# Kernel tuning notes

Hardware: AMD Instinct MI355X
Metric: run time of the kernel (lower is better)

Reference implementation:

```python
import jax, jax.numpy as jnp
import numpy as np

B, T, DIM = 4, 1024, 2048
N_HEADS, N_KV_HEADS = 32, 8
HEAD_DIM = DIM // N_HEADS  # 64
N_REPS = N_HEADS // N_KV_HEADS  # 4


def setup_inputs() -> dict:
    key = jax.random.key(0)
    ks = jax.random.split(key, 8)
    # RoPE tables: theta = 10000^{-2i/d}, positions 0..T-1
    inv_freq = 1.0 / (10000.0 ** (jnp.arange(0, HEAD_DIM, 2, dtype=jnp.float32) / HEAD_DIM))
    angles = jnp.arange(T, dtype=jnp.float32)[:, None] * inv_freq[None, :]  # (T, HEAD_DIM//2)
    s = 0.02
    return {
        "input": jax.random.normal(ks[0], (B, T, DIM), jnp.float32),
        "freqs_cos": jnp.cos(angles),
        "freqs_sin": jnp.sin(angles),
        "mask": jnp.tril(jnp.ones((T, T), dtype=bool)),  # causal boolean mask
        "wq": s * jax.random.normal(ks[1], (DIM, DIM), jnp.float32),
        "wk": s * jax.random.normal(ks[2], (N_KV_HEADS * HEAD_DIM, DIM), jnp.float32),
        "wv": s * jax.random.normal(ks[3], (N_KV_HEADS * HEAD_DIM, DIM), jnp.float32),
        "wo": s * jax.random.normal(ks[4], (DIM, DIM), jnp.float32),
        "curr_pos": 0,
    }


def _apply_rope(x, cos, sin):
    # x: (B, T, H, D); cos/sin: (T, D//2). Complex multiply on (even, odd) pairs.
    xr = x[..., 0::2]
    xi = x[..., 1::2]
    c = cos[None, :, None, :]
    s = sin[None, :, None, :]
    out_r = xr * c - xi * s
    out_i = xr * s + xi * c
    return jnp.stack([out_r, out_i], axis=-1).reshape(x.shape)


def reference(input, freqs_cos, freqs_sin, mask, wq, wk, wv, wo, curr_pos):
    Bv, Tv = input.shape[0], input.shape[1]
    qs = (input @ wq.T).reshape(Bv, Tv, N_HEADS, HEAD_DIM)
    ks = (input @ wk.T).reshape(Bv, Tv, N_KV_HEADS, HEAD_DIM)
    vs = (input @ wv.T).reshape(Bv, Tv, N_KV_HEADS, HEAD_DIM)
    qs = _apply_rope(qs, freqs_cos, freqs_sin)
    ks = _apply_rope(ks, freqs_cos, freqs_sin)

    # KV cache (prefill path: curr_pos == 0, fresh cache of length 2T)
    kv_cache = jnp.zeros((Bv, 2 * Tv, N_KV_HEADS, HEAD_DIM, 2), input.dtype)
    kv_cache = kv_cache.at[:, curr_pos:curr_pos + Tv, :, :, 0].set(ks)
    kv_cache = kv_cache.at[:, curr_pos:curr_pos + Tv, :, :, 1].set(vs)
    k_all = kv_cache[:, :curr_pos + Tv, :, :, 0]
    v_all = kv_cache[:, :curr_pos + Tv, :, :, 1]

    # GQA: broadcast each kv head across its query-head group (avoid repeat_interleave copy)
    S = k_all.shape[1]
    q = qs.transpose(0, 2, 1, 3).reshape(Bv, N_KV_HEADS, N_REPS, Tv, HEAD_DIM)
    k = k_all.transpose(0, 2, 1, 3)  # (B, KVH, S, D)
    v = v_all.transpose(0, 2, 1, 3)

    scale = 1.0 / jnp.sqrt(jnp.asarray(HEAD_DIM, input.dtype))
    scores = jnp.einsum("bgrqd,bgkd->bgrqk", q, k) * scale  # (B, KVH, REPS, T, S)
    neg = jnp.asarray(jnp.finfo(input.dtype).min, input.dtype)
    scores = jnp.where(mask[None, None, None, :, :S], scores, neg)
    attn = jax.nn.softmax(scores, axis=-1)
    out = jnp.einsum("bgrqk,bgkd->bgrqd", attn, v)
    out = out.reshape(Bv, N_HEADS, Tv, HEAD_DIM).transpose(0, 2, 1, 3).reshape(Bv, Tv, DIM)
    return out @ wo.T
```

## Files before the change

kernel.cpp:

```cpp
#include <hip/hip_runtime.h>
#include <cstdint>

typedef __bf16 bf16x8 __attribute__((ext_vector_type(8)));
typedef float  f32x4  __attribute__((ext_vector_type(4)));
typedef float  f32x16 __attribute__((ext_vector_type(16)));
typedef float  float8v __attribute__((ext_vector_type(8)));
typedef unsigned short ushort8v __attribute__((ext_vector_type(8)));
typedef unsigned short ushort4v __attribute__((ext_vector_type(4)));
typedef unsigned int   uint4v   __attribute__((ext_vector_type(4)));

__device__ __forceinline__ unsigned short f2b(float f) {
  uint32_t u = __builtin_bit_cast(uint32_t, f);
  u += 0x7FFFu + ((u >> 16) & 1u);
  return (unsigned short)(u >> 16);
}
__device__ __forceinline__ float b2f(unsigned short h) {
  uint32_t u = ((uint32_t)h) << 16;
  return __builtin_bit_cast(float, u);
}
__device__ __forceinline__ unsigned int cvtpk(float lo, float hi_) {
  unsigned int r;
  asm("v_cvt_pk_bf16_f32 %0, %1, %2" : "=v"(r) : "v"(lo), "v"(hi_));
  return r;
}

__device__ __forceinline__ void async16(const void* g, void* l) {
  __builtin_amdgcn_global_load_lds(
      (const __attribute__((address_space(1))) void*)g,
      (__attribute__((address_space(3))) void*)l, 16, 0, 0);
}

#define WAITVM(N)  __builtin_amdgcn_s_waitcnt(0x0F70 | ((N) & 15))
#define WAITLGKM0  __builtin_amdgcn_s_waitcnt(0xC07F)

struct CvtArgs {
  const float* src[5];
  unsigned short* dst[5];
  long n[5];
};
__global__ void cvt5_kernel(CvtArgs a) {
  long base = (long)blockIdx.x * blockDim.x + threadIdx.x;
  long gstride = (long)gridDim.x * blockDim.x;
#pragma unroll 1
  for (int sg = 0; sg < 5; ++sg) {
    const float* s = a.src[sg];
    unsigned short* d = a.dst[sg];
    long n8 = a.n[sg] >> 3;
    for (long i = base; i < n8; i += gstride) {
      float8v f = *(const float8v*)(s + i * 8);
      ushort8v o;
#pragma unroll
      for (int j = 0; j < 8; ++j) o[j] = f2b(f[j]);
      *(ushort8v*)(d + i * 8) = o;
    }
  }
}

template<bool F32OUT, int BN, int GX>
__global__ __launch_bounds__(512, 1)
void gemm8p(const unsigned short* __restrict__ Ag, const unsigned short* __restrict__ Wg,
            void* __restrict__ Cp, int M, int N) {
  constexpr int K = 2048;
  constexpr int NF = BN / 64;
  constexpr int BL = BN / 128;
  constexpr int VN = 4 + 2 * BL;
  constexpr int VT1 = (BN == 256) ? 6 : 4;
  constexpr int VT2 = (BN == 256) ? 4 : 3;
  constexpr int VT3 = (BN == 256) ? 2 : 1;
  constexpr int ASLOT = 16384;
  constexpr int BSLOT = BN * 64;
  constexpr int CPX = 2 * GX;

  extern __shared__ char lds_c[];

  const int tid = threadIdx.x;
  const int wave = tid >> 6, lane = tid & 63;
  const int wm = wave >> 2, wn = wave & 3;
  const int lr = lane & 15, lg = lane >> 4;

  const int flat = blockIdx.y * GX + blockIdx.x;
  const int swz = (flat & 7) * CPX + (flat >> 3);
  const int m0 = (swz / GX) * 256, n0 = (swz % GX) * BN;

  const int laneSw = (lr >> 1) * 128 + (((((lr & 1) << 2) | lg) ^ (lr >> 1)) << 4);
  const int aoff = wm * 8192 + laneSw;
  const int boff = wn * NF * 1024 + laneSw;

  f32x4 acc[8][NF] = {};

  auto stageHT = [&](int s) {
    const int ty = s & 3;
    const int kh = (s >> 1) & 1;
    const int buf = (s >> 2) & 1;
    const int kc = (s >> 2) * 64 + kh * 32;
    if (ty == 0 || ty == 2) {
      char* slot = lds_c + (buf * 2 + kh) * ASLOT;
#pragma unroll
      for (int j = 0; j < 2; ++j) {
        int q = (tid + 512 * j) * 16;
        int R = q >> 7, g2L = ((q >> 4) & 7) ^ (R & 7);
        int row = R * 2 + (g2L >> 2), kg = g2L & 3;
        async16(Ag + (size_t)(m0 + row) * K + kc + kg * 8, slot + q);
      }
    } else {
      char* slot = lds_c + 65536 + (buf * 2 + kh) * BSLOT;
#pragma unroll
      for (int j = 0; j < BL; ++j) {
        int q = (tid + 512 * j) * 16;
        int R = q >> 7, g2L = ((q >> 4) & 7) ^ (R & 7);
        int row = R * 2 + (g2L >> 2), kg = g2L & 3;
        async16(Wg + (size_t)(n0 + row) * K + kc + kg * 8, slot + q);
      }
    }
  };

#define PHASE(BUF, KH, MH, VM, ...)                                           \
  {                                                                           \
    const char* As_ = lds_c + ((BUF) * 2 + (KH)) * ASLOT;                     \
    const char* Bs_ = lds_c + 65536 + ((BUF) * 2 + (KH)) * BSLOT;             \
    bf16x8 af_[4], bf_[NF];                                                   \
    _Pragma("unroll") for (int mi = 0; mi < 4; ++mi)                          \
      af_[mi] = *(const bf16x8*)(As_ + aoff + (MH) * 4096 + mi * 1024);       \
    _Pragma("unroll") for (int ni = 0; ni < NF; ++ni)                         \
      bf_[ni] = *(const bf16x8*)(Bs_ + boff + ni * 1024);                     \
    __VA_ARGS__;                                                              \
    WAITVM(VM);                                                               \
    __builtin_amdgcn_s_barrier();                                             \
    WAITLGKM0;                                                                \
    __builtin_amdgcn_sched_barrier(0);                                        \
    __builtin_amdgcn_s_setprio(1);                                            \
    _Pragma("unroll") for (int mi = 0; mi < 4; ++mi)                          \
      _Pragma("unroll") for (int ni = 0; ni < NF; ++ni)                       \
        acc[(MH) * 4 + mi][ni] = __builtin_amdgcn_mfma_f32_16x16x32_bf16(     \
            af_[mi], bf_[ni], acc[(MH) * 4 + mi][ni], 0, 0, 0);               \
    __builtin_amdgcn_s_setprio(0);                                            \
    __builtin_amdgcn_s_barrier();                                             \
  }

#pragma unroll
  for (int s = 0; s < 6; ++s) stageHT(s);
  WAITVM(VN);
  __builtin_amdgcn_s_barrier();

#pragma unroll 2
  for (int kt = 0; kt < 30; ++kt) {
    const int buf = kt & 1;
    const int s0 = kt * 4 + 6;
    PHASE(buf, 0, 0, VN, stageHT(s0));
    PHASE(buf, 0, 1, VN, stageHT(s0 + 1));
    PHASE(buf, 1, 0, VN, stageHT(s0 + 2));
    PHASE(buf, 1, 1, VN, stageHT(s0 + 3));
  }
  PHASE(0, 0, 0, VN, stageHT(126));
  PHASE(0, 0, 1, VN, stageHT(127));
  PHASE(0, 1, 0, VT1, (void)0);
  PHASE(0, 1, 1, VT2, (void)0);
  PHASE(1, 0, 0, VT3, (void)0);
  PHASE(1, 0, 1, 0, (void)0);
  PHASE(1, 1, 0, 0, (void)0);
  PHASE(1, 1, 1, 0, (void)0);
#undef PHASE

#pragma unroll
  for (int mig = 0; mig < 8; ++mig) {
#pragma unroll
    for (int j = 0; j < 4; ++j) {
      int row = m0 + wm * 128 + mig * 16 + lg * 4 + j;
#pragma unroll
      for (int ni = 0; ni < NF; ++ni) {
        int col = n0 + wn * (NF * 16) + ni * 16 + lr;
        float v = acc[mig][ni][j];
        if (F32OUT) ((float*)Cp)[(size_t)row * N + col] = v;
        else        ((unsigned short*)Cp)[(size_t)row * N + col] = f2b(v);
      }
    }
  }
}

__global__ __launch_bounds__(256)
void ropekv_kernel(unsigned short* __restrict__ qkv,
                   const float* __restrict__ cosb, const float* __restrict__ sinb,
                   unsigned short* __restrict__ vt) {
  const int tt0 = blockIdx.x * 64;
  const int kvh = blockIdx.y;
  const int b   = blockIdx.z;
  const int tid = threadIdx.x;

  {
    int r = tid >> 2, c0 = (tid & 3) * 16;
    int t = tt0 + r;
    unsigned short* kp = qkv + (size_t)(b * 1024 + t) * 3072 + 2048 + kvh * 64 + c0;
    const float* cb = cosb + t * 32 + c0 / 2;
    const float* sb = sinb + t * 32 + c0 / 2;
    ushort8v x0 = *(const ushort8v*)kp;
    ushort8v x1 = *(const ushort8v*)(kp + 8);
    float8v c = *(const float8v*)cb;
    float8v s = *(const float8v*)sb;
    ushort8v o0, o1;
#pragma unroll
    for (int j = 0; j < 4; ++j) {
      float xr = b2f(x0[2 * j]), xi = b2f(x0[2 * j + 1]);
      o0[2 * j]     = f2b(xr * c[j] - xi * s[j]);
      o0[2 * j + 1] = f2b(xr * s[j] + xi * c[j]);
    }
#pragma unroll
    for (int j = 0; j < 4; ++j) {
      float xr = b2f(x1[2 * j]), xi = b2f(x1[2 * j + 1]);
      o1[2 * j]     = f2b(xr * c[4 + j] - xi * s[4 + j]);
      o1[2 * j + 1] = f2b(xr * s[4 + j] + xi * c[4 + j]);
    }
    *(ushort8v*)kp = o0;
    *(ushort8v*)(kp + 8) = o1;
  }

  __shared__ unsigned short lT[64 * 68];
#pragma unroll
  for (int i = 0; i < 2; ++i) {
    int r = i * 32 + (tid >> 3), c = (tid & 7) * 8;
    const unsigned short* src = qkv + (size_t)(b * 1024 + tt0 + r) * 3072 + 2560 + kvh * 64 + c;
    ushort8v v = *(const ushort8v*)src;
    ushort4v a, b4;
#pragma unroll
    for (int j = 0; j < 4; ++j) { a[j] = v[j]; b4[j] = v[j + 4]; }
    *(ushort4v*)&lT[r * 68 + c]     = a;
    *(ushort4v*)&lT[r * 68 + c + 4] = b4;
  }
  __syncthreads();
#pragma unroll
  for (int i = 0; i < 2; ++i) {
    int d = tid & 63;
    int tt = i * 4 + (tid >> 6);
    ushort8v o;
#pragma unroll
    for (int j = 0; j < 8; ++j) o[j] = lT[(tt * 8 + j) * 68 + d];
    *(ushort8v*)&vt[((size_t)((b * 8 + kvh) * 64 + d)) * 1024 + tt0 + tt * 8] = o;
  }
}

__global__ __launch_bounds__(256, 2)
void attn_kernel(const unsigned short* __restrict__ qkv, const unsigned short* __restrict__ vt,
                 const float* __restrict__ cosb, const float* __restrict__ sinb,
                 unsigned short* __restrict__ ob) {
  const int flat = (blockIdx.z * 8 + blockIdx.y) * 16 + blockIdx.x;
  const int swzb = (flat & 7) * 64 + (flat >> 3);
  const int bx = swzb & 15, kvh = (swzb >> 4) & 7, b = swzb >> 7;

  const int tid = threadIdx.x, wave = tid >> 6, lane = tid & 63;
  const int l31 = lane & 31, hi = lane >> 5;
  const int h = kvh * 4 + wave;

  const int qth = 31 - bx, qtl = bx;
  const int q0h = qth * 32, q0l = qtl * 32;
  const int nth = qth / 4 + 1, ntl = qtl / 4 + 1;

  __shared__ unsigned short lK[2][128 * 64];
  __shared__ unsigned short lVt[2][64 * 128];

  bf16x8 qfh[4], qfl[4];
  {
    auto ldq = [&](int q0, bf16x8* qf) {
      int t = q0 + l31;
      const unsigned short* qp = qkv + (size_t)(b * 1024 + t) * 3072 + h * 64;
#pragma unroll
      for (int dk = 0; dk < 4; ++dk) {
        ushort8v q = *(const ushort8v*)(qp + dk * 16 + hi * 8);
        f32x4 c4 = *(const f32x4*)(cosb + t * 32 + dk * 8 + hi * 4);
        f32x4 s4 = *(const f32x4*)(sinb + t * 32 + dk * 8 + hi * 4);
        ushort8v o;
#pragma unroll
        for (int j = 0; j < 4; ++j) {
          float xr = b2f(q[2 * j]), xi = b2f(q[2 * j + 1]);
          o[2 * j]     = f2b(xr * c4[j] - xi * s4[j]);
          o[2 * j + 1] = f2b(xr * s4[j] + xi * c4[j]);
        }
        qf[dk] = __builtin_bit_cast(bf16x8, o);
      }
    };
    ldq(q0h, qfh);
    ldq(q0l, qfl);
  }

  f32x16 oh[2] = {}, ol[2] = {};
  float mh = -3e38f, lh = 0.f, ml = -3e38f, ll = 0.f;

  const unsigned short* kg = qkv + (size_t)(b * 1024) * 3072 + 2048 + kvh * 64;
  const unsigned short* vg = vt + (size_t)(b * 8 + kvh) * 64 * 1024;

  auto stage = [&](int it, int bi) {
    const int kvb = it * 128;
    const int sr  = tid >> 3;
    const int scb = (tid & 7) * 16;
#pragma unroll
    for (int i = 0; i < 4; ++i) {
      int r = i * 32 + sr;
      int cb = scb ^ ((r & 7) << 4);
      async16(kg + (size_t)(kvb + r) * 3072 + (cb >> 1), &lK[bi][r * 64 + (scb >> 1)]);
    }
    const int rv0 = tid >> 4;
    const int scv = (tid & 15) * 16;
#pragma unroll
    for (int i = 0; i < 4; ++i) {
      int rv = i * 16 + rv0;
      int cbv = scv ^ ((rv & 15) << 4);
      async16(vg + (size_t)rv * 1024 + kvb + (cbv >> 1), &lVt[bi][rv * 128 + (scv >> 1)]);
    }
  };

  const float SC = 0.125f * 1.44269504f;
  auto state = [&](int cur, int kvb, bf16x8 (&qf)[4], float& m2, float& l_run,
                   f32x16 (&oacc)[2], int q0, bool last) {
    f32x16 sd[4] = {};
    __builtin_amdgcn_s_setprio(1);
#pragma unroll
    for (int s = 0; s < 4; ++s) {
      const int krow = s * 32 + l31;
      const char* kr = (const char*)lK[cur] + krow * 128;
      const int swz = (krow & 7) << 4;
#pragma unroll
      for (int dk = 0; dk < 4; ++dk) {
        bf16x8 kf = *(const bf16x8*)(kr + ((dk * 32 + hi * 16) ^ swz));
        sd[s] = __builtin_amdgcn_mfma_f32_32x32x16_bf16(kf, qf[dk], sd[s], 0, 0, 0);
      }
    }
    __builtin_amdgcn_s_setprio(0);

#pragma unroll
    for (int s = 0; s < 4; ++s)
#pragma unroll
      for (int r = 0; r < 16; ++r) {
        float v = sd[s][r] * SC;
        if (last) {
          int kvg = kvb + s * 32 + (r & 3) + 8 * (r >> 2) + 4 * hi;
          if (kvg > q0 + l31) v = -3e38f;
        }
        sd[s][r] = v;
      }
    float pm = sd[0][0];
#pragma unroll
    for (int s = 0; s < 4; ++s)
#pragma unroll
      for (int r = 0; r < 16; ++r) pm = fmaxf(pm, sd[s][r]);
    pm = fmaxf(pm, __shfl_xor(pm, 32));
    if (!__all(pm <= m2 + 11.0f)) {
      float mnew = fmaxf(m2, pm);
      float alpha = exp2f(m2 - mnew);
      m2 = mnew;
      l_run *= alpha;
#pragma unroll
      for (int db = 0; db < 2; ++db)
#pragma unroll
        for (int r = 0; r < 16; ++r) oacc[db][r] *= alpha;
    }
    float tsum = 0.f;
#pragma unroll
    for (int s = 0; s < 4; ++s)
#pragma unroll
      for (int r = 0; r < 16; ++r) { float p = exp2f(sd[s][r] - m2); sd[s][r] = p; tsum += p; }
    tsum += __shfl_xor(tsum, 32);
    l_run += tsum;

    bf16x8 pf[4][2];
#pragma unroll
    for (int s = 0; s < 4; ++s)
#pragma unroll
      for (int kc = 0; kc < 2; ++kc) {
        unsigned int cA = cvtpk(sd[s][8 * kc + 0], sd[s][8 * kc + 1]);
        unsigned int cB = cvtpk(sd[s][8 * kc + 4], sd[s][8 * kc + 5]);
        unsigned int cC = cvtpk(sd[s][8 * kc + 2], sd[s][8 * kc + 3]);
        unsigned int cD = cvtpk(sd[s][8 * kc + 6], sd[s][8 * kc + 7]);
        unsigned int xA = __shfl_xor(cA, 32), xB = __shfl_xor(cB, 32);
        unsigned int xC = __shfl_xor(cC, 32), xD = __shfl_xor(cD, 32);
        uint4v u;
        u[0] = hi ? xB : cA;
        u[1] = hi ? xD : cC;
        u[2] = hi ? cB : xA;
        u[3] = hi ? cD : xC;
        pf[s][kc] = __builtin_bit_cast(bf16x8, u);
      }

    __builtin_amdgcn_s_setprio(1);
#pragma unroll
    for (int db = 0; db < 2; ++db) {
      const int row = db * 32 + l31;
      const char* vr = (const char*)lVt[cur] + row * 256;
      const int vswz = (row & 15) << 4;
#pragma unroll
      for (int s = 0; s < 4; ++s)
#pragma unroll
        for (int kc = 0; kc < 2; ++kc) {
          bf16x8 vf = *(const bf16x8*)(vr + ((s * 64 + kc * 32 + hi * 16) ^ vswz));
          oacc[db] = __builtin_amdgcn_mfma_f32_32x32x16_bf16(vf, pf[s][kc], oacc[db], 0, 0, 0);
        }
    }
    __builtin_amdgcn_s_setprio(0);
  };

  stage(0, 0);
  __syncthreads();

  for (int it = 0; it < nth; ++it) {
    const int cur = it & 1;
    if (it + 1 < nth) stage(it + 1, cur ^ 1);
    const int kvb = it * 128;

    state(cur, kvb, qfh, mh, lh, oh, q0h, it == nth - 1);
    if (it < ntl) state(cur, kvb, qfl, ml, ll, ol, q0l, it == ntl - 1);

    __syncthreads();
  }

  {
    float inv = 1.0f / lh;
    unsigned short* orow = ob + (size_t)(b * 1024 + q0h + l31) * 2048 + h * 64;
#pragma unroll
    for (int db = 0; db < 2; ++db)
#pragma unroll
      for (int g = 0; g < 4; ++g) {
        int d0 = db * 32 + 8 * g + 4 * hi;
        ushort4v o;
#pragma unroll
        for (int j = 0; j < 4; ++j) o[j] = f2b(oh[db][4 * g + j] * inv);
        *(ushort4v*)(orow + d0) = o;
      }
  }
  {
    float inv = 1.0f / ll;
    unsigned short* orow = ob + (size_t)(b * 1024 + q0l + l31) * 2048 + h * 64;
#pragma unroll
    for (int db = 0; db < 2; ++db)
#pragma unroll
      for (int g = 0; g < 4; ++g) {
        int d0 = db * 32 + 8 * g + 4 * hi;
        ushort4v o;
#pragma unroll
        for (int j = 0; j < 4; ++j) o[j] = f2b(ol[db][4 * g + j] * inv);
        *(ushort4v*)(orow + d0) = o;
      }
  }
}

extern "C" void kernel_launch(void* const* d_in, const int* in_sizes, int n_in,
                              void* d_out, int out_size, void* d_ws, size_t ws_size,
                              hipStream_t stream) {
  const float* input = (const float*)d_in[0];
  const float* fcos  = (const float*)d_in[1];
  const float* fsin  = (const float*)d_in[2];
  const float* wq = (const float*)d_in[4];
  const float* wk = (const float*)d_in[5];
  const float* wv = (const float*)d_in[6];
  const float* wo = (const float*)d_in[7];
  float* out = (float*)d_out;

  unsigned short* xb   = (unsigned short*)d_ws;
  unsigned short* wqkv = xb + (size_t)4096 * 2048;
  unsigned short* wob  = wqkv + (size_t)3072 * 2048;
  unsigned short* qkv  = wob + (size_t)2048 * 2048;
  unsigned short* ob   = qkv + (size_t)4096 * 3072;
  unsigned short* vtb  = xb;

  hipFuncSetAttribute((const void*)&gemm8p<false, 256, 12>,
                      hipFuncAttributeMaxDynamicSharedMemorySize, 131072);
  hipFuncSetAttribute((const void*)&gemm8p<true, 128, 16>,
                      hipFuncAttributeMaxDynamicSharedMemorySize, 98304);

  CvtArgs ca;
  ca.src[0] = input; ca.dst[0] = xb;                        ca.n[0] = (long)4096 * 2048;
  ca.src[1] = wq;    ca.dst[1] = wqkv;                      ca.n[1] = (long)2048 * 2048;
  ca.src[2] = wk;    ca.dst[2] = wqkv + (size_t)2048 * 2048; ca.n[2] = (long)512 * 2048;
  ca.src[3] = wv;    ca.dst[3] = wqkv + (size_t)2560 * 2048; ca.n[3] = (long)512 * 2048;
  ca.src[4] = wo;    ca.dst[4] = wob;                       ca.n[4] = (long)2048 * 2048;
  hipLaunchKernelGGL(cvt5_kernel, dim3(2048), dim3(256), 0, stream, ca);

  hipLaunchKernelGGL((gemm8p<false, 256, 12>), dim3(12, 16), dim3(512), 131072,
                     stream, xb, wqkv, (void*)qkv, 4096, 3072);

  hipLaunchKernelGGL(ropekv_kernel, dim3(16, 8, 4), dim3(256), 0, stream,
                     qkv, fcos, fsin, vtb);

  hipLaunchKernelGGL(attn_kernel, dim3(16, 8, 4), dim3(256), 0, stream,
                     qkv, vtb, fcos, fsin, ob);

  hipLaunchKernelGGL((gemm8p<true, 128, 16>), dim3(16, 16), dim3(512), 98304,
                     stream, ob, wob, (void*)out, 4096, 2048);
}
```

Measured before the change: 185.3 us.

## Serialize paired query tiles and skip fully-masked 64-key chunks in attention

The attention kernel now handles its two query tiles one after another instead of interleaving them. Each one keeps a single set of accumulators, and the KV tiles are restaged for the low tile. Work inside each 128-key tile is split into 64-key chunks, and chunks lying entirely above the causal diagonal are skipped. This is meant to cut register pressure and avoid wasted MFMA and exp work on masked keys. In exchange the shared K/V tiles of the low query block are loaded twice, and there are more loop iterations and barriers.

```diff
diff --git a/kernel.cpp b/kernel.cpp
--- a/kernel.cpp
+++ b/kernel.cpp
@@ -252,42 +252,34 @@
   const int qth = 31 - bx, qtl = bx;
   const int q0h = qth * 32, q0l = qtl * 32;
   const int nth = qth / 4 + 1, ntl = qtl / 4 + 1;
+  const int ntot = nth + ntl;
 
   __shared__ unsigned short lK[2][128 * 64];
   __shared__ unsigned short lVt[2][64 * 128];
 
-  bf16x8 qfh[4], qfl[4];
-  {
-    auto ldq = [&](int q0, bf16x8* qf) {
-      int t = q0 + l31;
-      const unsigned short* qp = qkv + (size_t)(b * 1024 + t) * 3072 + h * 64;
-#pragma unroll
-      for (int dk = 0; dk < 4; ++dk) {
-        ushort8v q = *(const ushort8v*)(qp + dk * 16 + hi * 8);
-        f32x4 c4 = *(const f32x4*)(cosb + t * 32 + dk * 8 + hi * 4);
-        f32x4 s4 = *(const f32x4*)(sinb + t * 32 + dk * 8 + hi * 4);
-        ushort8v o;
-#pragma unroll
-        for (int j = 0; j < 4; ++j) {
-          float xr = b2f(q[2 * j]), xi = b2f(q[2 * j + 1]);
-          o[2 * j]     = f2b(xr * c4[j] - xi * s4[j]);
-          o[2 * j + 1] = f2b(xr * s4[j] + xi * c4[j]);
-        }
-        qf[dk] = __builtin_bit_cast(bf16x8, o);
-      }
-    };
-    ldq(q0h, qfh);
-    ldq(q0l, qfl);
-  }
-
-  f32x16 oh[2] = {}, ol[2] = {};
-  float mh = -3e38f, lh = 0.f, ml = -3e38f, ll = 0.f;
+  auto ldq = [&](int q0, bf16x8* qf) {
+    int t = q0 + l31;
+    const unsigned short* qp = qkv + (size_t)(b * 1024 + t) * 3072 + h * 64;
+#pragma unroll
+    for (int dk = 0; dk < 4; ++dk) {
+      ushort8v q = *(const ushort8v*)(qp + dk * 16 + hi * 8);
+      f32x4 c4 = *(const f32x4*)(cosb + t * 32 + dk * 8 + hi * 4);
+      f32x4 s4 = *(const f32x4*)(sinb + t * 32 + dk * 8 + hi * 4);
+      ushort8v o;
+#pragma unroll
+      for (int j = 0; j < 4; ++j) {
+        float xr = b2f(q[2 * j]), xi = b2f(q[2 * j + 1]);
+        o[2 * j]     = f2b(xr * c4[j] - xi * s4[j]);
+        o[2 * j + 1] = f2b(xr * s4[j] + xi * c4[j]);
+      }
+      qf[dk] = __builtin_bit_cast(bf16x8, o);
+    }
+  };
 
   const unsigned short* kg = qkv + (size_t)(b * 1024) * 3072 + 2048 + kvh * 64;
   const unsigned short* vg = vt + (size_t)(b * 8 + kvh) * 64 * 1024;
 
-  auto stage = [&](int it, int bi) {
-    const int kvb = it * 128;
+  auto stage = [&](int kvb, int bi) {
     const int sr  = tid >> 3;
     const int scb = (tid & 7) * 16;
 #pragma unroll
@@ -306,14 +298,21 @@
     }
   };
 
+  bf16x8 qf[4];
+  f32x16 oacc[2] = {};
+  float m2 = -3e38f, l_run = 0.f;
+  int q0 = q0h;
+
+  ldq(q0h, qf);
+
   const float SC = 0.125f * 1.44269504f;
-  auto state = [&](int cur, int kvb, bf16x8 (&qf)[4], float& m2, float& l_run,
-                   f32x16 (&oacc)[2], int q0, bool last) {
-    f32x16 sd[4] = {};
+
+  auto chunk64 = [&](int cur, int ckvb, int c, bool lastT) {
+    f32x16 sd[2] = {};
     __builtin_amdgcn_s_setprio(1);
 #pragma unroll
-    for (int s = 0; s < 4; ++s) {
-      const int krow = s * 32 + l31;
+    for (int s = 0; s < 2; ++s) {
+      const int krow = c * 64 + s * 32 + l31;
       const char* kr = (const char*)lK[cur] + krow * 128;
       const int swz = (krow & 7) << 4;
 #pragma unroll
@@ -325,19 +324,19 @@
     __builtin_amdgcn_s_setprio(0);
 
 #pragma unroll
-    for (int s = 0; s < 4; ++s)
+    for (int s = 0; s < 2; ++s)
 #pragma unroll
       for (int r = 0; r < 16; ++r) {
         float v = sd[s][r] * SC;
-        if (last) {
-          int kvg = kvb + s * 32 + (r & 3) + 8 * (r >> 2) + 4 * hi;
+        if (lastT) {
+          int kvg = ckvb + s * 32 + (r & 3) + 8 * (r >> 2) + 4 * hi;
           if (kvg > q0 + l31) v = -3e38f;
         }
         sd[s][r] = v;
       }
     float pm = sd[0][0];
 #pragma unroll
-    for (int s = 0; s < 4; ++s)
+    for (int s = 0; s < 2; ++s)
 #pragma unroll
       for (int r = 0; r < 16; ++r) pm = fmaxf(pm, sd[s][r]);
     pm = fmaxf(pm, __shfl_xor(pm, 32));
@@ -353,15 +352,15 @@
     }
     float tsum = 0.f;
 #pragma unroll
-    for (int s = 0; s < 4; ++s)
+    for (int s = 0; s < 2; ++s)
 #pragma unroll
       for (int r = 0; r < 16; ++r) { float p = exp2f(sd[s][r] - m2); sd[s][r] = p; tsum += p; }
     tsum += __shfl_xor(tsum, 32);
     l_run += tsum;
 
-    bf16x8 pf[4][2];
-#pragma unroll
-    for (int s = 0; s < 4; ++s)
+    bf16x8 pf[2][2];
+#pragma unroll
+    for (int s = 0; s < 2; ++s)
 #pragma unroll
       for (int kc = 0; kc < 2; ++kc) {
         unsigned int cA = cvtpk(sd[s][8 * kc + 0], sd[s][8 * kc + 1]);
@@ -385,33 +384,19 @@
       const char* vr = (const char*)lVt[cur] + row * 256;
       const int vswz = (row & 15) << 4;
 #pragma unroll
-      for (int s = 0; s < 4; ++s)
+      for (int s = 0; s < 2; ++s)
 #pragma unroll
         for (int kc = 0; kc < 2; ++kc) {
-          bf16x8 vf = *(const bf16x8*)(vr + ((s * 64 + kc * 32 + hi * 16) ^ vswz));
+          bf16x8 vf = *(const bf16x8*)(vr + ((c * 128 + s * 64 + kc * 32 + hi * 16) ^ vswz));
           oacc[db] = __builtin_amdgcn_mfma_f32_32x32x16_bf16(vf, pf[s][kc], oacc[db], 0, 0, 0);
         }
     }
     __builtin_amdgcn_s_setprio(0);
   };
 
-  stage(0, 0);
-  __syncthreads();
-
-  for (int it = 0; it < nth; ++it) {
-    const int cur = it & 1;
-    if (it + 1 < nth) stage(it + 1, cur ^ 1);
-    const int kvb = it * 128;
-
-    state(cur, kvb, qfh, mh, lh, oh, q0h, it == nth - 1);
-    if (it < ntl) state(cur, kvb, qfl, ml, ll, ol, q0l, it == ntl - 1);
-
-    __syncthreads();
-  }
-
-  {
-    float inv = 1.0f / lh;
-    unsigned short* orow = ob + (size_t)(b * 1024 + q0h + l31) * 2048 + h * 64;
+  auto writeOut = [&](int q0w) {
+    float inv = 1.0f / l_run;
+    unsigned short* orow = ob + (size_t)(b * 1024 + q0w + l31) * 2048 + h * 64;
 #pragma unroll
     for (int db = 0; db < 2; ++db)
 #pragma unroll
@@ -419,24 +404,38 @@
         int d0 = db * 32 + 8 * g + 4 * hi;
         ushort4v o;
 #pragma unroll
-        for (int j = 0; j < 4; ++j) o[j] = f2b(oh[db][4 * g + j] * inv);
+        for (int j = 0; j < 4; ++j) o[j] = f2b(oacc[db][4 * g + j] * inv);
         *(ushort4v*)(orow + d0) = o;
       }
-  }
-  {
-    float inv = 1.0f / ll;
-    unsigned short* orow = ob + (size_t)(b * 1024 + q0l + l31) * 2048 + h * 64;
-#pragma unroll
-    for (int db = 0; db < 2; ++db)
-#pragma unroll
-      for (int g = 0; g < 4; ++g) {
-        int d0 = db * 32 + 8 * g + 4 * hi;
-        ushort4v o;
-#pragma unroll
-        for (int j = 0; j < 4; ++j) o[j] = f2b(ol[db][4 * g + j] * inv);
-        *(ushort4v*)(orow + d0) = o;
-      }
-  }
+  };
+
+  auto kvb_of = [&](int j) { return (j < nth ? j : j - nth) * 128; };
+
+  stage(0, 0);
+  __syncthreads();
+
+  for (int j = 0; j < ntot; ++j) {
+    const int cur = j & 1;
+    if (j + 1 < ntot) stage(kvb_of(j + 1), cur ^ 1);
+    const int kvb = kvb_of(j);
+    const bool lastT = (j == nth - 1) || (j == ntot - 1);
+
+#pragma unroll 1
+    for (int c = 0; c < 2; ++c) {
+      if (kvb + c * 64 > q0 + 31) continue;
+      chunk64(cur, kvb + c * 64, c, lastT);
+    }
+
+    if (j == nth - 1) {
+      writeOut(q0h);
+      oacc[0] = f32x16{}; oacc[1] = f32x16{};
+      m2 = -3e38f; l_run = 0.f;
+      q0 = q0l;
+      ldq(q0l, qf);
+    }
+    __syncthreads();
+  }
+  writeOut(q0l);
 }
 
 extern "C" void kernel_launch(void* const* d_in, const int* in_sizes, int n_in,
```

Measured after the change: 171.2 us. 7.6% less time.
